# Optimization experiments

Measured on AMD Instinct MI355X. Metric: run time of the kernel, lower is better.

The kernel has to match this reference:

```python
import jax, jax.numpy as jnp
import numpy as np

H = 512  # hidden_dimension
B = 32
S = 2048


def setup_inputs() -> dict:
    key = jax.random.key(0)
    k1, k2, k3, k4, k5, k6 = jax.random.split(key, 6)
    decoder_hide = jax.random.normal(k1, (B, H), dtype=jnp.float32)
    encoder_out = jax.random.normal(k2, (B, S, 2 * H), dtype=jnp.float32)
    mask = jax.random.randint(k3, (B, S), 0, 2, dtype=jnp.int32)
    bound = 1.0 / np.sqrt(3 * H)
    W_attn = jax.random.uniform(k4, (3 * H, H), minval=-bound, maxval=bound, dtype=jnp.float32)
    b_attn = jax.random.uniform(k5, (H,), minval=-bound, maxval=bound, dtype=jnp.float32)
    bound_v = 1.0 / np.sqrt(H)
    v_w = jax.random.uniform(k6, (H,), minval=-bound_v, maxval=bound_v, dtype=jnp.float32)
    return {"decoder_hide": decoder_hide, "encoder_out": encoder_out, "mask": mask,
            "W_attn": W_attn, "b_attn": b_attn, "v_w": v_w}


def reference(decoder_hide, encoder_out, mask, W_attn, b_attn, v_w):
    # Split the concat-linear: cat((h, enc)) @ W == h @ W[:H] + enc @ W[H:]
    W_h = W_attn[:H]        # [H, H]
    W_e = W_attn[H:]        # [2H, H]
    dec_proj = decoder_hide @ W_h + b_attn                 # [B, H]
    enc_proj = jnp.einsum('bse,eh->bsh', encoder_out, W_e)  # [B, S, H]
    energy = jnp.tanh(enc_proj + dec_proj[:, None, :])      # [B, S, H]
    attention = jnp.einsum('bsh,h->bs', energy, v_w)        # [B, S]
    attention = jnp.where(mask == 0, jnp.float32(-100000.0), attention)
    return jax.nn.softmax(attention, axis=1)
```

## Files before the change

### kernel.cpp

```cpp
#include <hip/hip_runtime.h>
#include <hip/hip_bf16.h>
#include <math.h>

#define Hdim 512
#define Bdim 32
#define Sdim 2048
#define Kdim 1024
#define Mtot (Bdim * Sdim)

#define BM 64
#define BK 64

typedef __attribute__((ext_vector_type(8))) short short8;
typedef __attribute__((ext_vector_type(4))) float floatx4;

__device__ __forceinline__ short f2bf(float f) {
    union { float f; unsigned u; } v; v.f = f;
    unsigned r = v.u + 0x7fffu + ((v.u >> 16) & 1u);
    return (short)(r >> 16);
}

__device__ __forceinline__ short8 cvt8(float4 a, float4 b) {
    union { short8 s; __hip_bfloat162 h[4]; } u;
    u.h[0] = __float22bfloat162_rn(make_float2(a.x, a.y));
    u.h[1] = __float22bfloat162_rn(make_float2(a.z, a.w));
    u.h[2] = __float22bfloat162_rn(make_float2(b.x, b.y));
    u.h[3] = __float22bfloat162_rn(make_float2(b.z, b.w));
    return u.s;
}

__device__ __forceinline__ float fast_tanh(float x) {
    float ax = fabsf(x);
    float e  = __expf(-2.0f * ax);
    float r  = (1.0f - e) * __builtin_amdgcn_rcpf(1.0f + e);
    return copysignf(r, x);
}

__global__ __launch_bounds__(256) void prep_kernel(
    const float* __restrict__ W_attn, const float* __restrict__ dec,
    const float* __restrict__ b_attn, short* __restrict__ Wb,
    float* __restrict__ dec_proj)
{
    const int t = threadIdx.x;
    if (blockIdx.x < 512) {
        const float* We = W_attn + Hdim * Hdim;
        __shared__ short tile[32][33];
        const int k0 = (blockIdx.x >> 4) * 32;
        const int n0 = (blockIdx.x & 15) * 32;
        const int r = t >> 5, c = t & 31;
        #pragma unroll
        for (int rr = 0; rr < 4; ++rr)
            tile[r + rr * 8][c] = f2bf(We[(size_t)(k0 + r + rr * 8) * Hdim + n0 + c]);
        __syncthreads();
        #pragma unroll
        for (int rr = 0; rr < 4; ++rr)
            Wb[(size_t)(n0 + r + rr * 8) * Kdim + k0 + c] = tile[c][r + rr * 8];
    } else {
        __shared__ float partl[2][128];
        const int bid = blockIdx.x - 512;
        const int b  = bid >> 2;
        const int cb = bid & 3;
        const int c  = cb * 128 + (t & 127);
        const int kh = t >> 7;
        float acc = 0.0f;
        const int kbeg = kh * 256, kend = kbeg + 256;
        #pragma unroll 8
        for (int k = kbeg; k < kend; ++k)
            acc = fmaf(dec[b * Hdim + k], W_attn[(size_t)k * Hdim + c], acc);
        partl[kh][t & 127] = acc;
        __syncthreads();
        if (t < 128)
            dec_proj[b * Hdim + cb * 128 + t] = partl[0][t] + partl[1][t] + b_attn[cb * 128 + t];
    }
}

__global__ __launch_bounds__(512, 4) void scores_kernel(
    const float* __restrict__ enc,
    const short* __restrict__ Wb,
    const float* __restrict__ dec_proj,
    const float* __restrict__ v_w,
    float* __restrict__ scores)
{
    __shared__ __align__(16) short Asm[2 * BM * BK];
    __shared__ float redl[BM][8];

    const int t    = threadIdx.x;
    const int row0 = blockIdx.x * BM;
    const int b    = row0 / Sdim;

    const int w    = t >> 6;
    const int lane = t & 63;
    const int ln   = lane & 15;
    const int quad = lane >> 4;

    const int sm = t >> 3;
    const int sq = t & 7;
    const float* Ag = enc + (size_t)(row0 + sm) * Kdim + sq * 8;
    const int awo = sm * BK + ((sq ^ (sm & 7)) * 8);

    int arow[4];
    #pragma unroll
    for (int i = 0; i < 4; ++i) arow[i] = (i * 16 + ln) * BK;
    const int pf0 = (quad       ^ (ln & 7)) * 8;
    const int pf1 = ((4 + quad) ^ (ln & 7)) * 8;

    const short* Bl = Wb + (size_t)(w * 64 + ln) * Kdim + quad * 8;

    floatx4 acc[4][4];
    #pragma unroll
    for (int i = 0; i < 4; ++i)
        #pragma unroll
        for (int j = 0; j < 4; ++j)
            acc[i][j] = (floatx4)(0.0f);

    float4 ra0, ra1;
    {
        const float4* g = (const float4*)Ag;
        ra0 = g[0]; ra1 = g[1];
    }

    for (int kt = 0; kt < Kdim; kt += BK) {
        short* Ab = Asm + ((kt >> 6) & 1) * (BM * BK);
        *(short8*)&Ab[awo] = cvt8(ra0, ra1);
        __syncthreads();

        short8 b0[4], b1[4];
        #pragma unroll
        for (int j = 0; j < 4; ++j)
            b0[j] = *(const short8*)(Bl + (size_t)j * 16 * Kdim + kt);
        #pragma unroll
        for (int j = 0; j < 4; ++j)
            b1[j] = *(const short8*)(Bl + (size_t)j * 16 * Kdim + kt + 32);

        if (kt + BK < Kdim) {
            const float4* g = (const float4*)(Ag + kt + BK);
            ra0 = g[0]; ra1 = g[1];
        }

        short8 af[4];
        #pragma unroll
        for (int i = 0; i < 4; ++i) af[i] = *(const short8*)&Ab[arow[i] + pf0];
        #pragma unroll
        for (int i = 0; i < 4; ++i)
            #pragma unroll
            for (int j = 0; j < 4; ++j)
                acc[i][j] = __builtin_amdgcn_mfma_f32_16x16x32_bf16(
                                af[i], b0[j], acc[i][j], 0, 0, 0);
        #pragma unroll
        for (int i = 0; i < 4; ++i) af[i] = *(const short8*)&Ab[arow[i] + pf1];
        #pragma unroll
        for (int i = 0; i < 4; ++i)
            #pragma unroll
            for (int j = 0; j < 4; ++j)
                acc[i][j] = __builtin_amdgcn_mfma_f32_16x16x32_bf16(
                                af[i], b1[j], acc[i][j], 0, 0, 0);
    }

    float dpv[4], vwv[4];
    #pragma unroll
    for (int j = 0; j < 4; ++j) {
        int col = w * 64 + j * 16 + ln;
        dpv[j] = dec_proj[b * Hdim + col];
        vwv[j] = v_w[col];
    }
    #pragma unroll
    for (int i = 0; i < 4; ++i) {
        #pragma unroll
        for (int reg = 0; reg < 4; ++reg) {
            float s = 0.0f;
            #pragma unroll
            for (int j = 0; j < 4; ++j) {
                float x = acc[i][j][reg] + dpv[j];
                s = fmaf(vwv[j], fast_tanh(x), s);
            }
            s += __shfl_xor(s, 1, 64);
            s += __shfl_xor(s, 2, 64);
            s += __shfl_xor(s, 4, 64);
            s += __shfl_xor(s, 8, 64);
            if (ln == 0)
                redl[i * 16 + quad * 4 + reg][w] = s;
        }
    }
    __syncthreads();
    if (t < BM) {
        float s = 0.0f;
        #pragma unroll
        for (int wv = 0; wv < 8; ++wv) s += redl[t][wv];
        scores[row0 + t] = s;
    }
}

__global__ __launch_bounds__(256) void softmax_kernel(
    const float* __restrict__ scores, const int* __restrict__ mask,
    float* __restrict__ out)
{
    __shared__ float sred[8];
    const int b = blockIdx.x;
    const int t = threadIdx.x;
    const int lane = t & 63;
    const int wid  = t >> 6;

    float x[8];
    float m = -1e30f;
    #pragma unroll
    for (int j = 0; j < 8; ++j) {
        int idx = b * Sdim + j * 256 + t;
        float v = scores[idx];
        if (mask[idx] == 0) v = -100000.0f;
        x[j] = v;
        m = fmaxf(m, v);
    }
    #pragma unroll
    for (int off = 32; off >= 1; off >>= 1)
        m = fmaxf(m, __shfl_xor(m, off, 64));
    if (lane == 0) sred[wid] = m;
    __syncthreads();
    m = fmaxf(fmaxf(sred[0], sred[1]), fmaxf(sred[2], sred[3]));

    float s = 0.0f;
    #pragma unroll
    for (int j = 0; j < 8; ++j) {
        float e = __expf(x[j] - m);
        x[j] = e;
        s += e;
    }
    #pragma unroll
    for (int off = 32; off >= 1; off >>= 1)
        s += __shfl_xor(s, off, 64);
    if (lane == 0) sred[4 + wid] = s;
    __syncthreads();
    s = sred[4] + sred[5] + sred[6] + sred[7];

    const float inv = 1.0f / s;
    #pragma unroll
    for (int j = 0; j < 8; ++j)
        out[b * Sdim + j * 256 + t] = x[j] * inv;
}

extern "C" void kernel_launch(void* const* d_in, const int* in_sizes, int n_in,
                              void* d_out, int out_size, void* d_ws, size_t ws_size,
                              hipStream_t stream) {
    const float* dec  = (const float*)d_in[0];
    const float* enc  = (const float*)d_in[1];
    const int*   mask = (const int*)  d_in[2];
    const float* W    = (const float*)d_in[3];
    const float* ba   = (const float*)d_in[4];
    const float* vw   = (const float*)d_in[5];
    float* out = (float*)d_out;

    float* dec_proj = (float*)d_ws;
    short* Wb       = (short*)(dec_proj + Bdim * Hdim);
    float* scores   = (float*)(Wb + Hdim * Kdim);

    prep_kernel<<<640, 256, 0, stream>>>(W, dec, ba, Wb, dec_proj);
    scores_kernel<<<Mtot / BM, 512, 0, stream>>>(enc, Wb, dec_proj, vw, scores);
    softmax_kernel<<<Bdim, 256, 0, stream>>>(scores, mask, out);
}
```

Baseline: 450.7 us.

## Double K tile to 128 and prefetch encoder tiles two steps ahead

Increases the K tile of the scores GEMM from 64 to 128 and keeps two tiles of encoder activations in registers, so global loads are issued two iterations ahead of use. This halves the number of barriers and deepens the global-load pipeline to better hide HBM latency. It doubles LDS usage and adds registers for the prefetch buffers, which may reduce occupancy or cause spills under the existing launch bounds.

```diff
diff --git a/kernel.cpp b/kernel.cpp
--- a/kernel.cpp
+++ b/kernel.cpp
@@ -9,7 +9,7 @@
 #define Mtot (Bdim * Sdim)
 
 #define BM 64
-#define BK 64
+#define BK 128
 
 typedef __attribute__((ext_vector_type(8))) short short8;
 typedef __attribute__((ext_vector_type(4))) float floatx4;
@@ -96,13 +96,12 @@
     const int sm = t >> 3;
     const int sq = t & 7;
     const float* Ag = enc + (size_t)(row0 + sm) * Kdim + sq * 8;
-    const int awo = sm * BK + ((sq ^ (sm & 7)) * 8);
+    const int awo0 = sm * BK + ((sq       ^ (sm & 7)) * 8);
+    const int awo1 = sm * BK + (((sq + 8) ^ (sm & 7)) * 8);
 
     int arow[4];
     #pragma unroll
     for (int i = 0; i < 4; ++i) arow[i] = (i * 16 + ln) * BK;
-    const int pf0 = (quad       ^ (ln & 7)) * 8;
-    const int pf1 = ((4 + quad) ^ (ln & 7)) * 8;
 
     const short* Bl = Wb + (size_t)(w * 64 + ln) * Kdim + quad * 8;
 
@@ -113,47 +112,51 @@
         for (int j = 0; j < 4; ++j)
             acc[i][j] = (floatx4)(0.0f);
 
-    float4 ra0, ra1;
+    float4 ra[2][4];
     {
-        const float4* g = (const float4*)Ag;
-        ra0 = g[0]; ra1 = g[1];
-    }
-
-    for (int kt = 0; kt < Kdim; kt += BK) {
-        short* Ab = Asm + ((kt >> 6) & 1) * (BM * BK);
-        *(short8*)&Ab[awo] = cvt8(ra0, ra1);
+        const float4* g0 = (const float4*)Ag;
+        ra[0][0] = g0[0]; ra[0][1] = g0[1];
+        const float4* g0b = (const float4*)(Ag + 64);
+        ra[0][2] = g0b[0]; ra[0][3] = g0b[1];
+        const float4* g1 = (const float4*)(Ag + BK);
+        ra[1][0] = g1[0]; ra[1][1] = g1[1];
+        const float4* g1b = (const float4*)(Ag + BK + 64);
+        ra[1][2] = g1b[0]; ra[1][3] = g1b[1];
+    }
+
+    for (int i = 0; i < 8; ++i) {
+        const int kt = i << 7;
+        short* Ab = Asm + (i & 1) * (BM * BK);
+        *(short8*)&Ab[awo0] = cvt8(ra[i & 1][0], ra[i & 1][1]);
+        *(short8*)&Ab[awo1] = cvt8(ra[i & 1][2], ra[i & 1][3]);
         __syncthreads();
 
-        short8 b0[4], b1[4];
-        #pragma unroll
-        for (int j = 0; j < 4; ++j)
-            b0[j] = *(const short8*)(Bl + (size_t)j * 16 * Kdim + kt);
-        #pragma unroll
-        for (int j = 0; j < 4; ++j)
-            b1[j] = *(const short8*)(Bl + (size_t)j * 16 * Kdim + kt + 32);
-
-        if (kt + BK < Kdim) {
-            const float4* g = (const float4*)(Ag + kt + BK);
-            ra0 = g[0]; ra1 = g[1];
+        #pragma unroll
+        for (int p = 0; p < 4; ++p) {
+            short8 bfr[4];
+            #pragma unroll
+            for (int j = 0; j < 4; ++j)
+                bfr[j] = *(const short8*)(Bl + (size_t)j * 16 * Kdim + kt + p * 32);
+
+            if (p == 3 && i < 6) {
+                const float4* g  = (const float4*)(Ag + kt + 2 * BK);
+                ra[i & 1][0] = g[0]; ra[i & 1][1] = g[1];
+                const float4* gb = (const float4*)(Ag + kt + 2 * BK + 64);
+                ra[i & 1][2] = gb[0]; ra[i & 1][3] = gb[1];
+            }
+
+            const int pf = ((p * 4 + quad) ^ (ln & 7)) * 8;
+            short8 af[4];
+            #pragma unroll
+            for (int i2 = 0; i2 < 4; ++i2)
+                af[i2] = *(const short8*)&Ab[arow[i2] + pf];
+            #pragma unroll
+            for (int i2 = 0; i2 < 4; ++i2)
+                #pragma unroll
+                for (int j = 0; j < 4; ++j)
+                    acc[i2][j] = __builtin_amdgcn_mfma_f32_16x16x32_bf16(
+                                     af[i2], bfr[j], acc[i2][j], 0, 0, 0);
         }
-
-        short8 af[4];
-        #pragma unroll
-        for (int i = 0; i < 4; ++i) af[i] = *(const short8*)&Ab[arow[i] + pf0];
-        #pragma unroll
-        for (int i = 0; i < 4; ++i)
-            #pragma unroll
-            for (int j = 0; j < 4; ++j)
-                acc[i][j] = __builtin_amdgcn_mfma_f32_16x16x32_bf16(
-                                af[i], b0[j], acc[i][j], 0, 0, 0);
-        #pragma unroll
-        for (int i = 0; i < 4; ++i) af[i] = *(const short8*)&Ab[arow[i] + pf1];
-        #pragma unroll
-        for (int i = 0; i < 4; ++i)
-            #pragma unroll
-            for (int j = 0; j < 4; ++j)
-                acc[i][j] = __builtin_amdgcn_mfma_f32_16x16x32_bf16(
-                                af[i], b1[j], acc[i][j], 0, 0, 0);
     }
 
     float dpv[4], vwv[4];
```

New measurement: 467.5 us. 1.04x slower.
